# Kernel tuning notes

Hardware: AMD Instinct MI355X
Metric: run time of the kernel (lower is better)

Reference implementation:

```python
import jax, jax.numpy as jnp
import numpy as np


def setup_inputs() -> dict:
    key = jax.random.key(0)
    kq, kv = jax.random.split(key)
    N, To, Ti, H = 8, 1024, 4096, 512
    queries = jax.random.normal(kq, (N, To, H), dtype=jnp.float32)
    values = jax.random.normal(kv, (N, Ti, H), dtype=jnp.float32)
    return {"queries": queries, "values": values}


def reference(queries, values):
    # scores: N x To x Ti (unscaled, unmasked dot-product attention)
    scores = jnp.einsum("noh,nih->noi", queries, values)
    attn = jax.nn.softmax(scores, axis=-1)          # softmax over Ti
    out = jnp.einsum("noi,nih->noh", attn, values)  # N x To x H
    return out, attn
```

## Files before the change

kernel.cpp:

```cpp
#include <hip/hip_runtime.h>
#include <hip/hip_bf16.h>

typedef __bf16 bf16x8 __attribute__((ext_vector_type(8)));
typedef __bf16 bf16x4 __attribute__((ext_vector_type(4)));
typedef float  f32x4  __attribute__((ext_vector_type(4)));

constexpr int N_  = 8;
constexpr int TO_ = 1024;
constexpr int TI_ = 4096;
constexpr int H_  = 512;

__device__ inline void split8(const float4& x0, const float4& x1,
                              bf16x8& h, bf16x8& l)
{
    float xs[8] = {x0.x, x0.y, x0.z, x0.w, x1.x, x1.y, x1.z, x1.w};
#pragma unroll
    for (int i = 0; i < 8; ++i) {
        __bf16 hh = (__bf16)xs[i];
        h[i] = hh;
        l[i] = (__bf16)(xs[i] - (float)hh);
    }
}

__global__ __launch_bounds__(256)
void split_kernel(const float* __restrict__ X, __bf16* __restrict__ Xh,
                  __bf16* __restrict__ Xl)
{
    const size_t idx = ((size_t)blockIdx.x * 256 + threadIdx.x) * 8;
    const float4* src = reinterpret_cast<const float4*>(X + idx);
    float4 x0 = src[0], x1 = src[1];
    bf16x8 h, l;
    split8(x0, x1, h, l);
    *reinterpret_cast<bf16x8*>(Xh + idx) = h;
    *reinterpret_cast<bf16x8*>(Xl + idx) = l;
}

__global__ __launch_bounds__(256)
void splitv2_kernel(const float* __restrict__ V, __bf16* __restrict__ Vh,
                    __bf16* __restrict__ Vl, __bf16* __restrict__ Vt)
{
    __shared__ __bf16 Lh[64][72];

    const int tt = blockIdx.x, hb = blockIdx.y, n = blockIdx.z;
    const int t0 = tt * 64, h0 = hb * 64;
    const float* Vn = V + (size_t)n * TI_ * H_;
    __bf16* Vhn = Vh + (size_t)n * TI_ * H_;
    __bf16* Vln = Vl + (size_t)n * TI_ * H_;
    __bf16* Vtn = Vt + (size_t)n * H_ * TI_;

    const int tr = threadIdx.x >> 4;
    const int hc = (threadIdx.x & 15) * 4;

#pragma unroll
    for (int j = 0; j < 4; ++j) {
        const int t = tr + j * 16;
        const size_t o = (size_t)(t0 + t) * H_ + h0 + hc;
        float4 x = *reinterpret_cast<const float4*>(Vn + o);
        bf16x4 hv, lv;
        float xs[4] = {x.x, x.y, x.z, x.w};
#pragma unroll
        for (int e = 0; e < 4; ++e) {
            __bf16 hh = (__bf16)xs[e];
            hv[e] = hh;
            lv[e] = (__bf16)(xs[e] - (float)hh);
        }
        *reinterpret_cast<bf16x4*>(Vhn + o) = hv;
        *reinterpret_cast<bf16x4*>(Vln + o) = lv;
        *reinterpret_cast<bf16x4*>(&Lh[t][hc]) = hv;
    }
    __syncthreads();

    const int th = threadIdx.x >> 2;
    const int tq = threadIdx.x & 3;
#pragma unroll
    for (int s = 0; s < 2; ++s) {
        const int tb = tq * 16 + s * 8;
        bf16x8 o;
#pragma unroll
        for (int e = 0; e < 8; ++e) o[e] = Lh[tb + e][th];
        *reinterpret_cast<bf16x8*>(&Vtn[(size_t)(h0 + th) * TI_ + t0 + tb]) = o;
    }
}

__global__ __launch_bounds__(256, 2)
void qk3_kernel(const __bf16* __restrict__ Qh, const __bf16* __restrict__ Ql,
                const __bf16* __restrict__ Vh, const __bf16* __restrict__ Vl,
                float* __restrict__ S)
{
    __shared__ __bf16 Ah[128 * 64];
    __shared__ __bf16 Al[128 * 64];
    __shared__ __bf16 Bh[128 * 64];
    __shared__ __bf16 Bl[128 * 64];

    const int tt = blockIdx.x, mt = blockIdx.y, n = blockIdx.z;
    const size_t qoff = ((size_t)n * TO_ + (size_t)mt * 128) * H_;
    const size_t voff = ((size_t)n * TI_ + (size_t)tt * 128) * H_;
    const __bf16* Qhb = Qh + qoff;
    const __bf16* Qlb = Ql + qoff;
    const __bf16* Vhb = Vh + voff;
    const __bf16* Vlb = Vl + voff;

    const int tid  = threadIdx.x;
    const int lane = tid & 63, wave = tid >> 6;
    const int wr = wave >> 1, wc = wave & 1;
    const int fr = lane & 15, fq = lane >> 4;

    const int srow = tid >> 3;
    const int sc   = tid & 7;

    auto stage = [&](const __bf16* __restrict__ g, __bf16* lds, int k0) {
#pragma unroll
        for (int i = 0; i < 4; ++i) {
            const int row = i * 32 + srow;
            const int csw = sc ^ (row & 7);
            const __bf16* gs = g + (size_t)row * H_ + k0 + csw * 8;
            const int q0 = (i * 256 + wave * 64) * 16;
            __builtin_amdgcn_global_load_lds(
                (const __attribute__((address_space(1))) void*)gs,
                (__attribute__((address_space(3))) void*)((char*)lds + q0),
                16, 0, 0);
        }
    };

    f32x4 acc[4][4] = {};

    for (int kt = 0; kt < H_ / 64; ++kt) {
        const int k0 = kt * 64;
        __syncthreads();
        stage(Qhb, Ah, k0);
        stage(Qlb, Al, k0);
        stage(Vhb, Bh, k0);
        stage(Vlb, Bl, k0);
        __syncthreads();

#pragma unroll
        for (int kk = 0; kk < 2; ++kk) {
            bf16x8 ah[4], al[4], bh[4], bl[4];
#pragma unroll
            for (int m = 0; m < 4; ++m) {
                const int row = wr * 64 + m * 16 + fr;
                const int cs  = (kk * 4 + fq) ^ (row & 7);
                ah[m] = *reinterpret_cast<const bf16x8*>(&Ah[row * 64 + cs * 8]);
                al[m] = *reinterpret_cast<const bf16x8*>(&Al[row * 64 + cs * 8]);
            }
#pragma unroll
            for (int j = 0; j < 4; ++j) {
                const int row = wc * 64 + j * 16 + fr;
                const int cs  = (kk * 4 + fq) ^ (row & 7);
                bh[j] = *reinterpret_cast<const bf16x8*>(&Bh[row * 64 + cs * 8]);
                bl[j] = *reinterpret_cast<const bf16x8*>(&Bl[row * 64 + cs * 8]);
            }
#pragma unroll
            for (int m = 0; m < 4; ++m)
#pragma unroll
                for (int j = 0; j < 4; ++j) {
                    acc[m][j] = __builtin_amdgcn_mfma_f32_16x16x32_bf16(ah[m], bh[j], acc[m][j], 0, 0, 0);
                    acc[m][j] = __builtin_amdgcn_mfma_f32_16x16x32_bf16(ah[m], bl[j], acc[m][j], 0, 0, 0);
                    acc[m][j] = __builtin_amdgcn_mfma_f32_16x16x32_bf16(al[m], bh[j], acc[m][j], 0, 0, 0);
                }
        }
    }

    float* Sb = S + ((size_t)n * TO_ + (size_t)mt * 128) * TI_ + (size_t)tt * 128;
    const int crow0 = wr * 64 + fq * 4;
    const int ccol0 = wc * 64 + fr;
#pragma unroll
    for (int m = 0; m < 4; ++m)
#pragma unroll
        for (int j = 0; j < 4; ++j)
#pragma unroll
            for (int r = 0; r < 4; ++r)
                Sb[(size_t)(crow0 + m * 16 + r) * TI_ + (ccol0 + j * 16)] = acc[m][j][r];
}

__global__ __launch_bounds__(256)
void softmax2_kernel(float* __restrict__ S, __bf16* __restrict__ A16)
{
    const int wave = threadIdx.x >> 6, lane = threadIdx.x & 63;
    const size_t row = (size_t)blockIdx.x * 4 + wave;
    float4* p = reinterpret_cast<float4*>(S + row * TI_);
    __bf16* p16 = A16 + row * TI_;

    float4 v[16];
    float m = -3.0e38f;
#pragma unroll
    for (int j = 0; j < 16; ++j) {
        v[j] = p[j * 64 + lane];
        m = fmaxf(m, fmaxf(fmaxf(v[j].x, v[j].y), fmaxf(v[j].z, v[j].w)));
    }
#pragma unroll
    for (int s = 32; s > 0; s >>= 1) m = fmaxf(m, __shfl_xor(m, s));

    constexpr float L2E = 1.4426950408889634f;
    float sum = 0.f;
#pragma unroll
    for (int j = 0; j < 16; ++j) {
        v[j].x = exp2f((v[j].x - m) * L2E);
        v[j].y = exp2f((v[j].y - m) * L2E);
        v[j].z = exp2f((v[j].z - m) * L2E);
        v[j].w = exp2f((v[j].w - m) * L2E);
        sum += (v[j].x + v[j].y) + (v[j].z + v[j].w);
    }
#pragma unroll
    for (int s = 32; s > 0; s >>= 1) sum += __shfl_xor(sum, s);

    const float inv = 1.0f / sum;
#pragma unroll
    for (int j = 0; j < 16; ++j) {
        v[j].x *= inv; v[j].y *= inv; v[j].z *= inv; v[j].w *= inv;
        p[j * 64 + lane] = v[j];
        bf16x4 o;
        o[0] = (__bf16)v[j].x; o[1] = (__bf16)v[j].y;
        o[2] = (__bf16)v[j].z; o[3] = (__bf16)v[j].w;
        *reinterpret_cast<bf16x4*>(&p16[(j * 64 + lane) * 4]) = o;
    }
}

__global__ __launch_bounds__(512, 2)
void pv7_kernel(const __bf16* __restrict__ A16, const __bf16* __restrict__ Vt,
                float* __restrict__ O, float* __restrict__ P)
{
    __shared__ __bf16 AsmA[128 * 64], AsmB[128 * 64];
    __shared__ __bf16 BsmA[256 * 64], BsmB[256 * 64];

    const int flat = blockIdx.x;
    const int mt = flat >> 5;
    const int g  = flat & 31;
    const int n  = g >> 2;
    const int ht = (g >> 1) & 1;
    const int kc = g & 1;

    const __bf16* Ab = A16 + ((size_t)n * TO_ + (size_t)mt * 128) * TI_ + (size_t)kc * 2048;
    const __bf16* Bb = Vt  + ((size_t)n * H_  + (size_t)ht * 256) * TI_ + (size_t)kc * 2048;

    const int tid = threadIdx.x, lane = tid & 63, wave = tid >> 6;
    const int wm = wave >> 2, wh = wave & 3;
    const int fr = lane & 15, fq = lane >> 4;

    auto stage = [&](__bf16* asm_, __bf16* bsm_, int k0) {
#pragma unroll
        for (int i = 0; i < 2; ++i) {
            const int q   = i * 512 + tid;
            const int row = q >> 3, c = q & 7;
            const int csw = c ^ (row & 7);
            const __bf16* gs = Ab + (size_t)row * TI_ + k0 + csw * 8;
            const int q0 = (i * 512 + wave * 64) * 16;
            __builtin_amdgcn_global_load_lds(
                (const __attribute__((address_space(1))) void*)gs,
                (__attribute__((address_space(3))) void*)((char*)asm_ + q0),
                16, 0, 0);
        }
#pragma unroll
        for (int i = 0; i < 4; ++i) {
            const int q   = i * 512 + tid;
            const int row = q >> 3, c = q & 7;
            const int csw = c ^ (row & 7);
            const __bf16* gs = Bb + (size_t)row * TI_ + k0 + csw * 8;
            const int q0 = (i * 512 + wave * 64) * 16;
            __builtin_amdgcn_global_load_lds(
                (const __attribute__((address_space(1))) void*)gs,
                (__attribute__((address_space(3))) void*)((char*)bsm_ + q0),
                16, 0, 0);
        }
    };

    f32x4 acc[4][4] = {};

    auto compute = [&](const __bf16* Asm, const __bf16* Bsm) {
#pragma unroll
        for (int kk = 0; kk < 2; ++kk) {
            bf16x8 a[4], b[4];
#pragma unroll
            for (int m = 0; m < 4; ++m) {
                const int row = wm * 64 + m * 16 + fr;
                const int cs  = (kk * 4 + fq) ^ (row & 7);
                a[m] = *reinterpret_cast<const bf16x8*>(&Asm[row * 64 + cs * 8]);
            }
#pragma unroll
            for (int j = 0; j < 4; ++j) {
                const int row = wh * 64 + j * 16 + fr;
                const int cs  = (kk * 4 + fq) ^ (row & 7);
                b[j] = *reinterpret_cast<const bf16x8*>(&Bsm[row * 64 + cs * 8]);
            }
#pragma unroll
            for (int m = 0; m < 4; ++m)
#pragma unroll
                for (int j = 0; j < 4; ++j)
                    acc[m][j] = __builtin_amdgcn_mfma_f32_16x16x32_bf16(
                        a[m], b[j], acc[m][j], 0, 0, 0);
        }
    };

    constexpr int NT = 2048 / 64;
    stage(AsmA, BsmA, 0);
    __syncthreads();
    for (int kt = 0; kt < NT; kt += 2) {
        if (kt + 1 < NT) stage(AsmB, BsmB, (kt + 1) * 64);
        compute(AsmA, BsmA);
        __syncthreads();
        if (kt + 2 < NT) stage(AsmA, BsmA, (kt + 2) * 64);
        compute(AsmB, BsmB);
        __syncthreads();
    }

    float* D  = (kc == 0) ? O : P;
    float* Db = D + ((size_t)n * TO_ + (size_t)mt * 128) * H_ + ht * 256;
#pragma unroll
    for (int m = 0; m < 4; ++m) {
        const int orow = wm * 64 + m * 16 + fq * 4;
#pragma unroll
        for (int j = 0; j < 4; ++j) {
            const int ocol = wh * 64 + j * 16 + fr;
#pragma unroll
            for (int r = 0; r < 4; ++r)
                Db[(size_t)(orow + r) * H_ + ocol] = acc[m][j][r];
        }
    }
}

__global__ __launch_bounds__(256)
void add_kernel(float4* __restrict__ o, const float4* __restrict__ p)
{
    const size_t i = (size_t)blockIdx.x * 256 + threadIdx.x;
    float4 a = o[i], b = p[i];
    a.x += b.x; a.y += b.y; a.z += b.z; a.w += b.w;
    o[i] = a;
}

constexpr int BM1 = 128, BN1 = 128, BK1 = 32, LP1 = BK1 + 8;

__global__ __launch_bounds__(256, 2)
void qk_kernel(const float* __restrict__ Q, const float* __restrict__ V,
               float* __restrict__ S)
{
    __shared__ __bf16 Ah[BM1 * LP1];
    __shared__ __bf16 Al[BM1 * LP1];
    __shared__ __bf16 Bh[BN1 * LP1];
    __shared__ __bf16 Bl[BN1 * LP1];

    const int tt = blockIdx.x, mt = blockIdx.y, n = blockIdx.z;
    const float* Qb = Q + ((size_t)n * TO_ + (size_t)mt * BM1) * H_;
    const float* Vb = V + ((size_t)n * TI_ + (size_t)tt * BN1) * H_;

    const int tid  = threadIdx.x;
    const int lane = tid & 63, wave = tid >> 6;
    const int wr = wave >> 1, wc = wave & 1;
    const int srow = tid >> 2, scg = tid & 3;

    f32x4 acc[4][4] = {};

    for (int k0 = 0; k0 < H_; k0 += BK1) {
        __syncthreads();
#pragma unroll
        for (int half = 0; half < 2; ++half) {
            const int r = srow + half * 64;
            {
                const float4* src =
                    reinterpret_cast<const float4*>(Qb + (size_t)r * H_ + k0 + scg * 8);
                float4 x0 = src[0], x1 = src[1];
                bf16x8 hv, lv;
                split8(x0, x1, hv, lv);
                *reinterpret_cast<bf16x8*>(&Ah[r * LP1 + scg * 8]) = hv;
                *reinterpret_cast<bf16x8*>(&Al[r * LP1 + scg * 8]) = lv;
            }
            {
                const float4* src =
                    reinterpret_cast<const float4*>(Vb + (size_t)r * H_ + k0 + scg * 8);
                float4 x0 = src[0], x1 = src[1];
                bf16x8 hv, lv;
                split8(x0, x1, hv, lv);
                *reinterpret_cast<bf16x8*>(&Bh[r * LP1 + scg * 8]) = hv;
                *reinterpret_cast<bf16x8*>(&Bl[r * LP1 + scg * 8]) = lv;
            }
        }
        __syncthreads();

        bf16x8 ah[4], al[4], bh[4], bl[4];
        const int fr = lane & 15, fg = (lane >> 4) * 8;
#pragma unroll
        for (int m = 0; m < 4; ++m) {
            const int row = wr * 64 + m * 16 + fr;
            ah[m] = *reinterpret_cast<const bf16x8*>(&Ah[row * LP1 + fg]);
            al[m] = *reinterpret_cast<const bf16x8*>(&Al[row * LP1 + fg]);
        }
#pragma unroll
        for (int j = 0; j < 4; ++j) {
            const int row = wc * 64 + j * 16 + fr;
            bh[j] = *reinterpret_cast<const bf16x8*>(&Bh[row * LP1 + fg]);
            bl[j] = *reinterpret_cast<const bf16x8*>(&Bl[row * LP1 + fg]);
        }
#pragma unroll
        for (int m = 0; m < 4; ++m)
#pragma unroll
            for (int j = 0; j < 4; ++j) {
                acc[m][j] = __builtin_amdgcn_mfma_f32_16x16x32_bf16(ah[m], bh[j], acc[m][j], 0, 0, 0);
                acc[m][j] = __builtin_amdgcn_mfma_f32_16x16x32_bf16(ah[m], bl[j], acc[m][j], 0, 0, 0);
                acc[m][j] = __builtin_amdgcn_mfma_f32_16x16x32_bf16(al[m], bh[j], acc[m][j], 0, 0, 0);
            }
    }

    float* Sb = S + ((size_t)n * TO_ + (size_t)mt * BM1) * TI_ + (size_t)tt * BN1;
    const int crow0 = wr * 64 + (lane >> 4) * 4;
    const int ccol0 = wc * 64 + (lane & 15);
#pragma unroll
    for (int m = 0; m < 4; ++m)
#pragma unroll
        for (int j = 0; j < 4; ++j)
#pragma unroll
            for (int r = 0; r < 4; ++r)
                Sb[(size_t)(crow0 + m * 16 + r) * TI_ + (ccol0 + j * 16)] = acc[m][j][r];
}

__global__ __launch_bounds__(256)
void softmax_kernel(float* __restrict__ S)
{
    const int wave = threadIdx.x >> 6, lane = threadIdx.x & 63;
    const size_t row = (size_t)blockIdx.x * 4 + wave;
    float4* p = reinterpret_cast<float4*>(S + row * TI_);

    float4 v[16];
    float m = -3.0e38f;
#pragma unroll
    for (int j = 0; j < 16; ++j) {
        v[j] = p[j * 64 + lane];
        m = fmaxf(m, fmaxf(fmaxf(v[j].x, v[j].y), fmaxf(v[j].z, v[j].w)));
    }
#pragma unroll
    for (int s = 32; s > 0; s >>= 1) m = fmaxf(m, __shfl_xor(m, s));

    constexpr float L2E = 1.4426950408889634f;
    float sum = 0.f;
#pragma unroll
    for (int j = 0; j < 16; ++j) {
        v[j].x = exp2f((v[j].x - m) * L2E);
        v[j].y = exp2f((v[j].y - m) * L2E);
        v[j].z = exp2f((v[j].z - m) * L2E);
        v[j].w = exp2f((v[j].w - m) * L2E);
        sum += (v[j].x + v[j].y) + (v[j].z + v[j].w);
    }
#pragma unroll
    for (int s = 32; s > 0; s >>= 1) sum += __shfl_xor(sum, s);

    const float inv = 1.0f / sum;
#pragma unroll
    for (int j = 0; j < 16; ++j) {
        v[j].x *= inv; v[j].y *= inv; v[j].z *= inv; v[j].w *= inv;
        p[j * 64 + lane] = v[j];
    }
}

__global__ __launch_bounds__(256)
void vt_kernel(const float* __restrict__ V, __bf16* __restrict__ Vt)
{
    const int hb = blockIdx.x, tb = blockIdx.y, n = blockIdx.z;
    const int h  = hb * 64 + (threadIdx.x >> 2);
    const int tq = threadIdx.x & 3;
    const float* Vn = V + (size_t)n * TI_ * H_;
    __bf16* Vtn = Vt + (size_t)n * H_ * TI_;

#pragma unroll
    for (int j = 0; j < 16; ++j) {
        const int t0 = tb * 512 + tq * 128 + j * 8;
        bf16x8 o;
#pragma unroll
        for (int e = 0; e < 8; ++e)
            o[e] = (__bf16)Vn[(size_t)(t0 + e) * H_ + h];
        *reinterpret_cast<bf16x8*>(&Vtn[(size_t)h * TI_ + t0]) = o;
    }
}

constexpr int PBM = 32, PBK = 64, PLP = PBK + 8;

__global__ __launch_bounds__(512, 2)
void pv_fast_kernel(const float* __restrict__ A, const __bf16* __restrict__ Vt,
                    float* __restrict__ O)
{
    __shared__ __bf16 AsmF[PBM * PLP];
    __shared__ __bf16 BsmF[512 * PLP];

    const int n = blockIdx.x, mt = blockIdx.y;
    const float*  Ab = A  + ((size_t)n * TO_ + (size_t)mt * PBM) * TI_;
    const __bf16* Vb = Vt + (size_t)n * H_ * TI_;

    const int tid = threadIdx.x, lane = tid & 63, wv = tid >> 6;
    const int ar = tid >> 4;
    const int ac = (tid & 15) * 4;
    const int bh = tid >> 3;
    const int bc = (tid & 7) * 8;

    float4 aReg;
    bf16x8 bReg[8];

    auto loadTile = [&](int k0) {
        aReg = *reinterpret_cast<const float4*>(Ab + (size_t)ar * TI_ + k0 + ac);
#pragma unroll
        for (int i = 0; i < 8; ++i)
            bReg[i] = *reinterpret_cast<const bf16x8*>(
                Vb + (size_t)(bh + i * 64) * TI_ + k0 + bc);
    };

    f32x4 acc[2][4] = {};
    const int fr = lane & 15, fg = (lane >> 4) * 8;

    loadTile(0);
    constexpr int NT = TI_ / PBK;
    for (int kt = 0; kt < NT; ++kt) {
        __syncthreads();
        {
            bf16x4 av;
            av[0] = (__bf16)aReg.x; av[1] = (__bf16)aReg.y;
            av[2] = (__bf16)aReg.z; av[3] = (__bf16)aReg.w;
            *reinterpret_cast<bf16x4*>(&AsmF[ar * PLP + ac]) = av;
#pragma unroll
            for (int i = 0; i < 8; ++i)
                *reinterpret_cast<bf16x8*>(&BsmF[(bh + i * 64) * PLP + bc]) = bReg[i];
        }
        __syncthreads();
        if (kt + 1 < NT) loadTile((kt + 1) * PBK);

#pragma unroll
        for (int kk = 0; kk < 2; ++kk) {
            bf16x8 af[2], bfr[4];
#pragma unroll
            for (int m = 0; m < 2; ++m)
                af[m] = *reinterpret_cast<const bf16x8*>(
                    &AsmF[(m * 16 + fr) * PLP + kk * 32 + fg]);
#pragma unroll
            for (int j = 0; j < 4; ++j)
                bfr[j] = *reinterpret_cast<const bf16x8*>(
                    &BsmF[(wv * 64 + j * 16 + fr) * PLP + kk * 32 + fg]);
#pragma unroll
            for (int m = 0; m < 2; ++m)
#pragma unroll
                for (int j = 0; j < 4; ++j)
                    acc[m][j] = __builtin_amdgcn_mfma_f32_16x16x32_bf16(
                        af[m], bfr[j], acc[m][j], 0, 0, 0);
        }
    }

    float* Ob = O + ((size_t)n * TO_ + (size_t)mt * PBM) * H_ + wv * 64;
    const int crow = (lane >> 4) * 4;
    const int ccol = lane & 15;
#pragma unroll
    for (int m = 0; m < 2; ++m)
#pragma unroll
        for (int j = 0; j < 4; ++j)
#pragma unroll
            for (int r = 0; r < 4; ++r)
                Ob[(size_t)(m * 16 + crow + r) * H_ + j * 16 + ccol] = acc[m][j][r];
}

extern "C" void kernel_launch(void* const* d_in, const int* in_sizes, int n_in,
                              void* d_out, int out_size, void* d_ws, size_t ws_size,
                              hipStream_t stream)
{
    const float* Q = (const float*)d_in[0];
    const float* V = (const float*)d_in[1];
    float* out  = (float*)d_out;
    float* attn = out + (size_t)N_ * TO_ * H_;

    const size_t NV = (size_t)N_ * TI_ * H_;
    const size_t NQ = (size_t)N_ * TO_ * H_;
    const size_t FULL_BYTES = (3 * NV + 2 * NQ) * sizeof(__bf16);
    const size_t VT_BYTES   = NV * sizeof(__bf16);

    __bf16* wsb = (__bf16*)d_ws;
    __bf16* Vt = wsb;
    __bf16* Vh = wsb + NV;
    __bf16* Vl = wsb + 2 * NV;
    __bf16* Qh = wsb + 3 * NV;
    __bf16* Ql = wsb + 3 * NV + NQ;
    __bf16* A16 = wsb + NV;
    float*  Ppart = (float*)(wsb + 3 * NV);

    if (ws_size >= FULL_BYTES) {
        splitv2_kernel<<<dim3(TI_ / 64, H_ / 64, N_), 256, 0, stream>>>(V, Vh, Vl, Vt);
        split_kernel<<<dim3(NQ / (256 * 8)), 256, 0, stream>>>(Q, Qh, Ql);
        qk3_kernel<<<dim3(TI_ / 128, TO_ / 128, N_), 256, 0, stream>>>(Qh, Ql, Vh, Vl, attn);
        softmax2_kernel<<<dim3(N_ * TO_ / 4), 256, 0, stream>>>(attn, A16);
        pv7_kernel<<<dim3(256), 512, 0, stream>>>(A16, Vt, out, Ppart);
        add_kernel<<<dim3((unsigned)(NQ / 4 / 256)), 256, 0, stream>>>(
            (float4*)out, (const float4*)Ppart);
    } else if (ws_size >= VT_BYTES) {
        vt_kernel<<<dim3(H_ / 64, TI_ / 512, N_), 256, 0, stream>>>(V, Vt);
        qk_kernel<<<dim3(TI_ / BN1, TO_ / BM1, N_), 256, 0, stream>>>(Q, V, attn);
        softmax_kernel<<<dim3(N_ * TO_ / 4), 256, 0, stream>>>(attn);
        pv_fast_kernel<<<dim3(N_, TO_ / PBM), 512, 0, stream>>>(attn, Vt, out);
    }
}
```

Before: 249.0 us.

## Use 32x32 MFMA in QK and drop split-K partial sums in PV

The QK kernel switches from 16x16x32 to 32x32x16 bf16 MFMA tiles, so each wave issues fewer, larger matrix ops over the same 64x64 output per wave. The PV kernel stops splitting the Ti reduction in two halves. Instead it halves the M tile to 64 rows and loops over the full Ti, which removes the partial-sum buffer and the separate add kernel. The trade-off is longer per-block reduction loops and less A reuse per block in PV. The QK epilogue also gets a different store pattern.

```diff
diff --git a/kernel.cpp b/kernel.cpp
--- a/kernel.cpp
+++ b/kernel.cpp
@@ -4,6 +4,7 @@
 typedef __bf16 bf16x8 __attribute__((ext_vector_type(8)));
 typedef __bf16 bf16x4 __attribute__((ext_vector_type(4)));
 typedef float  f32x4  __attribute__((ext_vector_type(4)));
+typedef float  f32x16 __attribute__((ext_vector_type(16)));
 
 constexpr int N_  = 8;
 constexpr int TO_ = 1024;
@@ -83,9 +84,9 @@
 }
 
 __global__ __launch_bounds__(256, 2)
-void qk3_kernel(const __bf16* __restrict__ Qh, const __bf16* __restrict__ Ql,
-                const __bf16* __restrict__ Vh, const __bf16* __restrict__ Vl,
-                float* __restrict__ S)
+void qk32_kernel(const __bf16* __restrict__ Qh, const __bf16* __restrict__ Ql,
+                 const __bf16* __restrict__ Vh, const __bf16* __restrict__ Vl,
+                 float* __restrict__ S)
 {
     __shared__ __bf16 Ah[128 * 64];
     __shared__ __bf16 Al[128 * 64];
@@ -103,7 +104,7 @@
     const int tid  = threadIdx.x;
     const int lane = tid & 63, wave = tid >> 6;
     const int wr = wave >> 1, wc = wave & 1;
-    const int fr = lane & 15, fq = lane >> 4;
+    const int fr32 = lane & 31, kh = lane >> 5;
 
     const int srow = tid >> 3;
     const int sc   = tid & 7;
@@ -122,7 +123,7 @@
         }
     };
 
-    f32x4 acc[4][4] = {};
+    f32x16 acc[2][2] = {};
 
     for (int kt = 0; kt < H_ / 64; ++kt) {
         const int k0 = kt * 64;
@@ -134,43 +135,45 @@
         __syncthreads();
 
 #pragma unroll
-        for (int kk = 0; kk < 2; ++kk) {
-            bf16x8 ah[4], al[4], bh[4], bl[4];
-#pragma unroll
-            for (int m = 0; m < 4; ++m) {
-                const int row = wr * 64 + m * 16 + fr;
-                const int cs  = (kk * 4 + fq) ^ (row & 7);
+        for (int ks = 0; ks < 4; ++ks) {
+            bf16x8 ah[2], al[2], bh[2], bl[2];
+#pragma unroll
+            for (int m = 0; m < 2; ++m) {
+                const int row = wr * 64 + m * 32 + fr32;
+                const int cs  = (ks * 2 + kh) ^ (row & 7);
                 ah[m] = *reinterpret_cast<const bf16x8*>(&Ah[row * 64 + cs * 8]);
                 al[m] = *reinterpret_cast<const bf16x8*>(&Al[row * 64 + cs * 8]);
             }
 #pragma unroll
-            for (int j = 0; j < 4; ++j) {
-                const int row = wc * 64 + j * 16 + fr;
-                const int cs  = (kk * 4 + fq) ^ (row & 7);
+            for (int j = 0; j < 2; ++j) {
+                const int row = wc * 64 + j * 32 + fr32;
+                const int cs  = (ks * 2 + kh) ^ (row & 7);
                 bh[j] = *reinterpret_cast<const bf16x8*>(&Bh[row * 64 + cs * 8]);
                 bl[j] = *reinterpret_cast<const bf16x8*>(&Bl[row * 64 + cs * 8]);
             }
 #pragma unroll
-            for (int m = 0; m < 4; ++m)
-#pragma unroll
-                for (int j = 0; j < 4; ++j) {
-                    acc[m][j] = __builtin_amdgcn_mfma_f32_16x16x32_bf16(ah[m], bh[j], acc[m][j], 0, 0, 0);
-                    acc[m][j] = __builtin_amdgcn_mfma_f32_16x16x32_bf16(ah[m], bl[j], acc[m][j], 0, 0, 0);
-                    acc[m][j] = __builtin_amdgcn_mfma_f32_16x16x32_bf16(al[m], bh[j], acc[m][j], 0, 0, 0);
+            for (int m = 0; m < 2; ++m)
+#pragma unroll
+                for (int j = 0; j < 2; ++j) {
+                    acc[m][j] = __builtin_amdgcn_mfma_f32_32x32x16_bf16(ah[m], bh[j], acc[m][j], 0, 0, 0);
+                    acc[m][j] = __builtin_amdgcn_mfma_f32_32x32x16_bf16(ah[m], bl[j], acc[m][j], 0, 0, 0);
+                    acc[m][j] = __builtin_amdgcn_mfma_f32_32x32x16_bf16(al[m], bh[j], acc[m][j], 0, 0, 0);
                 }
         }
     }
 
     float* Sb = S + ((size_t)n * TO_ + (size_t)mt * 128) * TI_ + (size_t)tt * 128;
-    const int crow0 = wr * 64 + fq * 4;
-    const int ccol0 = wc * 64 + fr;
-#pragma unroll
-    for (int m = 0; m < 4; ++m)
-#pragma unroll
-        for (int j = 0; j < 4; ++j)
-#pragma unroll
-            for (int r = 0; r < 4; ++r)
-                Sb[(size_t)(crow0 + m * 16 + r) * TI_ + (ccol0 + j * 16)] = acc[m][j][r];
+#pragma unroll
+    for (int m = 0; m < 2; ++m)
+#pragma unroll
+        for (int j = 0; j < 2; ++j) {
+            const int col = wc * 64 + j * 32 + fr32;
+#pragma unroll
+            for (int r = 0; r < 16; ++r) {
+                const int row = wr * 64 + m * 32 + (r & 3) + 8 * (r >> 2) + 4 * kh;
+                Sb[(size_t)row * TI_ + col] = acc[m][j][r];
+            }
+        }
 }
 
 __global__ __launch_bounds__(256)
@@ -217,34 +220,31 @@
 }
 
 __global__ __launch_bounds__(512, 2)
-void pv7_kernel(const __bf16* __restrict__ A16, const __bf16* __restrict__ Vt,
-                float* __restrict__ O, float* __restrict__ P)
-{
-    __shared__ __bf16 AsmA[128 * 64], AsmB[128 * 64];
+void pv8b_kernel(const __bf16* __restrict__ A16, const __bf16* __restrict__ Vt,
+                 float* __restrict__ O)
+{
+    __shared__ __bf16 AsmA[64 * 64],  AsmB[64 * 64];
     __shared__ __bf16 BsmA[256 * 64], BsmB[256 * 64];
 
     const int flat = blockIdx.x;
-    const int mt = flat >> 5;
-    const int g  = flat & 31;
-    const int n  = g >> 2;
-    const int ht = (g >> 1) & 1;
-    const int kc = g & 1;
-
-    const __bf16* Ab = A16 + ((size_t)n * TO_ + (size_t)mt * 128) * TI_ + (size_t)kc * 2048;
-    const __bf16* Bb = Vt  + ((size_t)n * H_  + (size_t)ht * 256) * TI_ + (size_t)kc * 2048;
+    const int n  = flat & 7;
+    const int r  = flat >> 3;
+    const int mt = r >> 1;
+    const int ht = r & 1;
+
+    const __bf16* Ab = A16 + ((size_t)n * TO_ + (size_t)mt * 64) * TI_;
+    const __bf16* Bb = Vt  + ((size_t)n * H_  + (size_t)ht * 256) * TI_;
 
     const int tid = threadIdx.x, lane = tid & 63, wave = tid >> 6;
     const int wm = wave >> 2, wh = wave & 3;
     const int fr = lane & 15, fq = lane >> 4;
 
     auto stage = [&](__bf16* asm_, __bf16* bsm_, int k0) {
-#pragma unroll
-        for (int i = 0; i < 2; ++i) {
-            const int q   = i * 512 + tid;
-            const int row = q >> 3, c = q & 7;
+        {
+            const int row = tid >> 3, c = tid & 7;
             const int csw = c ^ (row & 7);
             const __bf16* gs = Ab + (size_t)row * TI_ + k0 + csw * 8;
-            const int q0 = (i * 512 + wave * 64) * 16;
+            const int q0 = (wave * 64) * 16;
             __builtin_amdgcn_global_load_lds(
                 (const __attribute__((address_space(1))) void*)gs,
                 (__attribute__((address_space(3))) void*)((char*)asm_ + q0),
@@ -264,15 +264,15 @@
         }
     };
 
-    f32x4 acc[4][4] = {};
+    f32x4 acc[2][4] = {};
 
     auto compute = [&](const __bf16* Asm, const __bf16* Bsm) {
 #pragma unroll
         for (int kk = 0; kk < 2; ++kk) {
-            bf16x8 a[4], b[4];
-#pragma unroll
-            for (int m = 0; m < 4; ++m) {
-                const int row = wm * 64 + m * 16 + fr;
+            bf16x8 a[2], b[4];
+#pragma unroll
+            for (int m = 0; m < 2; ++m) {
+                const int row = wm * 32 + m * 16 + fr;
                 const int cs  = (kk * 4 + fq) ^ (row & 7);
                 a[m] = *reinterpret_cast<const bf16x8*>(&Asm[row * 64 + cs * 8]);
             }
@@ -283,7 +283,7 @@
                 b[j] = *reinterpret_cast<const bf16x8*>(&Bsm[row * 64 + cs * 8]);
             }
 #pragma unroll
-            for (int m = 0; m < 4; ++m)
+            for (int m = 0; m < 2; ++m)
 #pragma unroll
                 for (int j = 0; j < 4; ++j)
                     acc[m][j] = __builtin_amdgcn_mfma_f32_16x16x32_bf16(
@@ -291,7 +291,7 @@
         }
     };
 
-    constexpr int NT = 2048 / 64;
+    constexpr int NT = TI_ / 64;
     stage(AsmA, BsmA, 0);
     __syncthreads();
     for (int kt = 0; kt < NT; kt += 2) {
@@ -303,28 +303,18 @@
         __syncthreads();
     }
 
-    float* D  = (kc == 0) ? O : P;
-    float* Db = D + ((size_t)n * TO_ + (size_t)mt * 128) * H_ + ht * 256;
-#pragma unroll
-    for (int m = 0; m < 4; ++m) {
-        const int orow = wm * 64 + m * 16 + fq * 4;
+    float* Ob = O + ((size_t)n * TO_ + (size_t)mt * 64) * H_ + ht * 256;
+#pragma unroll
+    for (int m = 0; m < 2; ++m) {
+        const int orow = wm * 32 + m * 16 + fq * 4;
 #pragma unroll
         for (int j = 0; j < 4; ++j) {
             const int ocol = wh * 64 + j * 16 + fr;
 #pragma unroll
-            for (int r = 0; r < 4; ++r)
-                Db[(size_t)(orow + r) * H_ + ocol] = acc[m][j][r];
-        }
-    }
-}
-
-__global__ __launch_bounds__(256)
-void add_kernel(float4* __restrict__ o, const float4* __restrict__ p)
-{
-    const size_t i = (size_t)blockIdx.x * 256 + threadIdx.x;
-    float4 a = o[i], b = p[i];
-    a.x += b.x; a.y += b.y; a.z += b.z; a.w += b.w;
-    o[i] = a;
+            for (int r2 = 0; r2 < 4; ++r2)
+                Ob[(size_t)(orow + r2) * H_ + ocol] = acc[m][j][r2];
+        }
+    }
 }
 
 constexpr int BM1 = 128, BN1 = 128, BK1 = 32, LP1 = BK1 + 8;
@@ -571,16 +561,13 @@
     __bf16* Qh = wsb + 3 * NV;
     __bf16* Ql = wsb + 3 * NV + NQ;
     __bf16* A16 = wsb + NV;
-    float*  Ppart = (float*)(wsb + 3 * NV);
 
     if (ws_size >= FULL_BYTES) {
         splitv2_kernel<<<dim3(TI_ / 64, H_ / 64, N_), 256, 0, stream>>>(V, Vh, Vl, Vt);
         split_kernel<<<dim3(NQ / (256 * 8)), 256, 0, stream>>>(Q, Qh, Ql);
-        qk3_kernel<<<dim3(TI_ / 128, TO_ / 128, N_), 256, 0, stream>>>(Qh, Ql, Vh, Vl, attn);
+        qk32_kernel<<<dim3(TI_ / 128, TO_ / 128, N_), 256, 0, stream>>>(Qh, Ql, Vh, Vl, attn);
         softmax2_kernel<<<dim3(N_ * TO_ / 4), 256, 0, stream>>>(attn, A16);
-        pv7_kernel<<<dim3(256), 512, 0, stream>>>(A16, Vt, out, Ppart);
-        add_kernel<<<dim3((unsigned)(NQ / 4 / 256)), 256, 0, stream>>>(
-            (float4*)out, (const float4*)Ppart);
+        pv8b_kernel<<<dim3(256), 512, 0, stream>>>(A16, Vt, out);
     } else if (ws_size >= VT_BYTES) {
         vt_kernel<<<dim3(H_ / 64, TI_ / 512, N_), 256, 0, stream>>>(V, Vt);
         qk_kernel<<<dim3(TI_ / BN1, TO_ / BM1, N_), 256, 0, stream>>>(Q, V, attn);
```

Measured after the change: 273.2 us. +9.7%, slower.
